# Performance work log

Measured on AMD Instinct MI355X. Metric: run time of the kernel, lower is better.

Reference implementation:

```python
import jax, jax.numpy as jnp
import numpy as np


def setup_inputs() -> dict:
    key = jax.random.key(0)
    kq, kk, kv = jax.random.split(key, 3)
    B, H, S, D = 2, 16, 2048, 128
    return {
        "query_states": jax.random.normal(kq, (B, H, S, D), dtype=jnp.float32),
        "key_states": jax.random.normal(kk, (B, H, S, D), dtype=jnp.float32),
        "value_states": jax.random.normal(kv, (B, H, S, D), dtype=jnp.float32),
    }


def reference(query_states, key_states, value_states):
    # Faithful translation of CoreAttention.forward with attention_mask=None,
    # attention_dropout=0.0 (default, and dropout with p=0 is identity).
    B, H, Sq, D = query_states.shape
    Skv = key_states.shape[-2]
    scale = 1.0 / jnp.sqrt(jnp.asarray(D, dtype=query_states.dtype))
    # [B,H,Sq,Skv] score matrix (the module materializes this explicitly)
    attn_weights = jnp.einsum("bhqd,bhkd->bhqk", query_states, key_states) * scale
    # internal causal mask: triu(ones, diagonal=1) positions -> dtype min
    causal = jnp.triu(jnp.ones((Sq, Skv), dtype=bool), k=1)
    mask_value = jnp.finfo(attn_weights.dtype).min
    attn_weights = jnp.where(causal[None, None], mask_value, attn_weights)
    # torch does softmax in float64 then casts back; numerically stable fp32
    # softmax is equivalent to working precision here (jax x64 disabled).
    attn_weights = jax.nn.softmax(attn_weights, axis=-1).astype(query_states.dtype)
    attn_output = jnp.einsum("bhqk,bhkd->bhqd", attn_weights, value_states)
    return attn_output
```

## Files before the change

### kernel.cpp

```cpp
#include <hip/hip_runtime.h>
#include <hip/hip_bf16.h>
#include <stdint.h>

typedef __bf16  bf16x8 __attribute__((ext_vector_type(8)));
typedef __bf16  bf16x4 __attribute__((ext_vector_type(4)));
typedef float   f32x4  __attribute__((ext_vector_type(4)));
typedef uint32_t u32x4 __attribute__((ext_vector_type(4)));

#define SLEN  2048
#define DHEAD 128
#define QBLK  64
#define KVBLK 32
#define NQT   (SLEN / QBLK)
#define THR   8.0f
#define VSTR  40

__device__ __forceinline__ uint32_t cvt_pk(float lo, float hi2) {
    uint32_t u;
    asm("v_cvt_pk_bf16_f32 %0, %1, %2" : "=v"(u) : "v"(lo), "v"(hi2));
    return u;
}

__global__ __launch_bounds__(256, 3) void attn_fwd(
    const float* __restrict__ Q, const float* __restrict__ K,
    const float* __restrict__ V, float* __restrict__ O)
{
    const int bh = blockIdx.x;
    const int qt = (NQT - 1) - blockIdx.y;
    const int tid  = threadIdx.x;
    const int w    = tid >> 6;
    const int lane = tid & 63;
    const int r    = lane & 15;
    const int g    = lane >> 4;

    const size_t head_off = (size_t)bh * SLEN * DHEAD;
    const float* Qh = Q + head_off;
    const float* Kh = K + head_off;
    const float* Vh = V + head_off;
    float*       Oh = O + head_off;

    const int q0w = qt * QBLK + w * 16;

    __shared__ __bf16 K_sh [2][KVBLK * DHEAD];
    __shared__ __bf16 Vt_sh[2][DHEAD * VSTR];

    const float scale = 0.08838834764831845f;

    bf16x8 qfrag[4];
    {
        const float4* qp = reinterpret_cast<const float4*>(
            Qh + (size_t)(q0w + r) * DHEAD + g * 8);
        #pragma unroll
        for (int kb = 0; kb < 4; ++kb) {
            float4 a = qp[kb*8 + 0];
            float4 b = qp[kb*8 + 1];
            a.x*=scale; a.y*=scale; a.z*=scale; a.w*=scale;
            b.x*=scale; b.y*=scale; b.z*=scale; b.w*=scale;
            bf16x8 f;
            f[0]=(__bf16)a.x; f[1]=(__bf16)a.y; f[2]=(__bf16)a.z; f[3]=(__bf16)a.w;
            f[4]=(__bf16)b.x; f[5]=(__bf16)b.y; f[6]=(__bf16)b.z; f[7]=(__bf16)b.w;
            qfrag[kb] = f;
        }
    }

    float4 kreg[4], vreg[4];
    const int c4  = tid & 31;
    const int kvq = tid >> 5;

    auto issue_loads = [&](int kv0) {
        #pragma unroll
        for (int it = 0; it < 4; ++it) {
            const int row = (it * 256 + tid) >> 5;
            kreg[it] = *reinterpret_cast<const float4*>(
                Kh + (size_t)(kv0 + row) * DHEAD + c4 * 4);
        }
        #pragma unroll
        for (int kr = 0; kr < 4; ++kr)
            vreg[kr] = *reinterpret_cast<const float4*>(
                Vh + (size_t)(kv0 + kvq * 4 + kr) * DHEAD + c4 * 4);
    };

    auto write_tiles = [&](int buf) {
        char* Kb  = reinterpret_cast<char*>(K_sh[buf]);
        char* Vtb = reinterpret_cast<char*>(Vt_sh[buf]);
        #pragma unroll
        for (int it = 0; it < 4; ++it) {
            const int row = (it * 256 + tid) >> 5;
            bf16x4 k4;
            k4[0]=(__bf16)kreg[it].x; k4[1]=(__bf16)kreg[it].y;
            k4[2]=(__bf16)kreg[it].z; k4[3]=(__bf16)kreg[it].w;
            *reinterpret_cast<bf16x4*>(
                Kb + row * 256 + ((c4 * 8) ^ ((row & 15) << 4))) = k4;
        }
        #pragma unroll
        for (int j = 0; j < 4; ++j) {
            const int d = c4 * 4 + j;
            bf16x4 v4;
            #pragma unroll
            for (int kr = 0; kr < 4; ++kr)
                v4[kr] = (__bf16)((&vreg[kr].x)[j]);
            *reinterpret_cast<bf16x4*>(
                Vtb + d * 80 + ((kvq ^ ((d >> 2) & 6)) * 8)) = v4;
        }
    };

    const f32x4 vzero = {0.f, 0.f, 0.f, 0.f};
    f32x4 acc_o[8];
    #pragma unroll
    for (int i = 0; i < 8; ++i) acc_o[i] = vzero;
    float m_run = -1e30f, l_run = 0.f;

    issue_loads(0);
    write_tiles(0);

    const int kvt_blk_max = 2 * qt + 1;
    const int kvt_max_w   = (q0w + 15) >> 5;
    int cur = 0;

    for (int kvt = 0; kvt <= kvt_blk_max; ++kvt) {
        __syncthreads();
        const bool more = (kvt < kvt_blk_max);
        if (more) issue_loads((kvt + 1) * KVBLK);

        if (kvt <= kvt_max_w) {
            const int kv0 = kvt * KVBLK;
            char* Kb  = reinterpret_cast<char*>(K_sh[cur]);
            char* Vtb = reinterpret_cast<char*>(Vt_sh[cur]);

            const bool alive1 = (kv0 + 16 <= q0w + 15);

            f32x4 st[2] = {vzero, vzero};
            __builtin_amdgcn_s_setprio(1);
            #pragma unroll
            for (int t = 0; t < 2; ++t) {
                if (t == 1 && !alive1) break;
                const int row = t * 16 + r;
                #pragma unroll
                for (int kb = 0; kb < 4; ++kb) {
                    bf16x8 kf = *reinterpret_cast<const bf16x8*>(
                        Kb + row * 256 + ((kb*64 + g*16) ^ ((row & 15) << 4)));
                    st[t] = __builtin_amdgcn_mfma_f32_16x16x32_bf16(
                        kf, qfrag[kb], st[t], 0, 0, 0);
                }
            }
            __builtin_amdgcn_s_setprio(0);

            const int q = q0w + r;
            float pmax = -1e30f;
            #pragma unroll
            for (int t = 0; t < 2; ++t) {
                if (t == 1 && !alive1) break;
                if (kv0 + t*16 + 15 > q0w) {
                    #pragma unroll
                    for (int j = 0; j < 4; ++j)
                        if (kv0 + t*16 + 4*g + j > q) st[t][j] = -1e30f;
                }
                #pragma unroll
                for (int j = 0; j < 4; ++j) pmax = fmaxf(pmax, st[t][j]);
            }
            pmax = fmaxf(pmax, __shfl_xor(pmax, 16));
            pmax = fmaxf(pmax, __shfl_xor(pmax, 32));

            if (__any(pmax > m_run + THR)) {
                const float m_new = fmaxf(m_run, pmax);
                const float corr  = __expf(m_run - m_new);
                l_run *= corr; m_run = m_new;
                #pragma unroll
                for (int reg = 0; reg < 4; ++reg) {
                    const float cr = __shfl(corr, 4*g + reg);
                    #pragma unroll
                    for (int dt = 0; dt < 8; ++dt) acc_o[dt][reg] *= cr;
                }
            }

            float rowsum = 0.f;
            #pragma unroll
            for (int t = 0; t < 2; ++t) {
                if (t == 1 && !alive1) break;
                #pragma unroll
                for (int j = 0; j < 4; ++j) {
                    const float p = __expf(st[t][j] - m_run);
                    st[t][j] = p;
                    rowsum += p;
                }
            }
            rowsum += __shfl_xor(rowsum, 16);
            rowsum += __shfl_xor(rowsum, 32);
            l_run += rowsum;

            const uint32_t p00 = cvt_pk(st[0][0], st[0][1]);
            const uint32_t p01 = cvt_pk(st[0][2], st[0][3]);
            const uint32_t p10 = alive1 ? cvt_pk(st[1][0], st[1][1]) : 0u;
            const uint32_t p11 = alive1 ? cvt_pk(st[1][2], st[1][3]) : 0u;
            const int sA = r + ((2 * (g & 1)) << 4);
            const int sB = r + ((2 * (g & 1) + 1) << 4);
            u32x4 words;
            {
                const uint32_t lo0 = (uint32_t)__shfl((int)p00, sA);
                const uint32_t hi0 = (uint32_t)__shfl((int)p10, sA);
                const uint32_t lo1 = (uint32_t)__shfl((int)p01, sA);
                const uint32_t hi1 = (uint32_t)__shfl((int)p11, sA);
                const uint32_t lo2 = (uint32_t)__shfl((int)p00, sB);
                const uint32_t hi2 = (uint32_t)__shfl((int)p10, sB);
                const uint32_t lo3 = (uint32_t)__shfl((int)p01, sB);
                const uint32_t hi3 = (uint32_t)__shfl((int)p11, sB);
                words[0] = (g & 2) ? hi0 : lo0;
                words[1] = (g & 2) ? hi1 : lo1;
                words[2] = (g & 2) ? hi2 : lo2;
                words[3] = (g & 2) ? hi3 : lo3;
            }
            const bf16x8 pa = __builtin_bit_cast(bf16x8, words);

            __builtin_amdgcn_s_setprio(1);
            #pragma unroll
            for (int dt = 0; dt < 8; ++dt) {
                const int d = dt * 16 + r;
                bf16x8 vf = *reinterpret_cast<const bf16x8*>(
                    Vtb + d * 80 + (((2*g) ^ ((d >> 2) & 6)) * 8));
                acc_o[dt] = __builtin_amdgcn_mfma_f32_16x16x32_bf16(
                    pa, vf, acc_o[dt], 0, 0, 0);
            }
            __builtin_amdgcn_s_setprio(0);
        }

        if (more) write_tiles(cur ^ 1);
        cur ^= 1;
    }

    const float inv = 1.0f / l_run;
    #pragma unroll
    for (int reg = 0; reg < 4; ++reg) {
        const float iv = __shfl(inv, 4*g + reg);
        float* orow = Oh + (size_t)(q0w + 4*g + reg) * DHEAD + r;
        #pragma unroll
        for (int dt = 0; dt < 8; ++dt)
            orow[dt * 16] = acc_o[dt][reg] * iv;
    }
}

extern "C" void kernel_launch(void* const* d_in, const int* in_sizes, int n_in,
                              void* d_out, int out_size, void* d_ws, size_t ws_size,
                              hipStream_t stream) {
    const float* Q = (const float*)d_in[0];
    const float* K = (const float*)d_in[1];
    const float* V = (const float*)d_in[2];
    float* O = (float*)d_out;
    dim3 grid(32 , NQT);
    attn_fwd<<<grid, 256, 0, stream>>>(Q, K, V, O);
}
```

Baseline: 92.46 us.

## Split KV range across two warp groups with 512-thread blocks and merge partial softmax

New measurement: 108.0 us. 16.8% more time.

```diff
diff --git a/kernel.cpp b/kernel.cpp
--- a/kernel.cpp
+++ b/kernel.cpp
@@ -10,10 +10,8 @@
 #define SLEN  2048
 #define DHEAD 128
 #define QBLK  64
-#define KVBLK 32
 #define NQT   (SLEN / QBLK)
 #define THR   8.0f
-#define VSTR  40
 
 __device__ __forceinline__ uint32_t cvt_pk(float lo, float hi2) {
     uint32_t u;
@@ -21,7 +19,7 @@
     return u;
 }
 
-__global__ __launch_bounds__(256, 3) void attn_fwd(
+__global__ __launch_bounds__(512, 4) void attn_fwd(
     const float* __restrict__ Q, const float* __restrict__ K,
     const float* __restrict__ V, float* __restrict__ O)
 {
@@ -29,6 +27,8 @@
     const int qt = (NQT - 1) - blockIdx.y;
     const int tid  = threadIdx.x;
     const int w    = tid >> 6;
+    const int tb   = w >> 2;
+    const int wq   = w & 3;
     const int lane = tid & 63;
     const int r    = lane & 15;
     const int g    = lane >> 4;
@@ -39,10 +39,10 @@
     const float* Vh = V + head_off;
     float*       Oh = O + head_off;
 
-    const int q0w = qt * QBLK + w * 16;
-
-    __shared__ __bf16 K_sh [2][KVBLK * DHEAD];
-    __shared__ __bf16 Vt_sh[2][DHEAD * VSTR];
+    const int q0w = qt * QBLK + wq * 16;
+
+    __shared__ __align__(16) char smem[65536];
+    __shared__ float ml_sh[4][16][2];
 
     const float scale = 0.08838834764831845f;
 
@@ -64,28 +64,28 @@
     }
 
     float4 kreg[4], vreg[4];
-    const int c4  = tid & 31;
-    const int kvq = tid >> 5;
+    const int c4 = tid & 31;
+    const int q6 = tid >> 5;
 
     auto issue_loads = [&](int kv0) {
         #pragma unroll
         for (int it = 0; it < 4; ++it) {
-            const int row = (it * 256 + tid) >> 5;
+            const int row = (it * 512 + tid) >> 5;
             kreg[it] = *reinterpret_cast<const float4*>(
                 Kh + (size_t)(kv0 + row) * DHEAD + c4 * 4);
         }
         #pragma unroll
         for (int kr = 0; kr < 4; ++kr)
             vreg[kr] = *reinterpret_cast<const float4*>(
-                Vh + (size_t)(kv0 + kvq * 4 + kr) * DHEAD + c4 * 4);
+                Vh + (size_t)(kv0 + q6 * 4 + kr) * DHEAD + c4 * 4);
     };
 
     auto write_tiles = [&](int buf) {
-        char* Kb  = reinterpret_cast<char*>(K_sh[buf]);
-        char* Vtb = reinterpret_cast<char*>(Vt_sh[buf]);
+        char* Kb  = smem + buf * 16384;
+        char* Vtb = smem + 32768 + buf * 16384;
         #pragma unroll
         for (int it = 0; it < 4; ++it) {
-            const int row = (it * 256 + tid) >> 5;
+            const int row = (it * 512 + tid) >> 5;
             bf16x4 k4;
             k4[0]=(__bf16)kreg[it].x; k4[1]=(__bf16)kreg[it].y;
             k4[2]=(__bf16)kreg[it].z; k4[3]=(__bf16)kreg[it].w;
@@ -99,8 +99,9 @@
             #pragma unroll
             for (int kr = 0; kr < 4; ++kr)
                 v4[kr] = (__bf16)((&vreg[kr].x)[j]);
+            const int slot16 = (q6 >> 1) ^ ((c4 + 2*j) & 7);
             *reinterpret_cast<bf16x4*>(
-                Vtb + d * 80 + ((kvq ^ ((d >> 2) & 6)) * 8)) = v4;
+                Vtb + d * 128 + (slot16 << 4) + ((q6 & 1) << 3)) = v4;
         }
     };
 
@@ -113,20 +114,17 @@
     issue_loads(0);
     write_tiles(0);
 
-    const int kvt_blk_max = 2 * qt + 1;
-    const int kvt_max_w   = (q0w + 15) >> 5;
+    const int n_iter = qt + 1;
     int cur = 0;
 
-    for (int kvt = 0; kvt <= kvt_blk_max; ++kvt) {
+    for (int i = 0; i < n_iter; ++i) {
         __syncthreads();
-        const bool more = (kvt < kvt_blk_max);
-        if (more) issue_loads((kvt + 1) * KVBLK);
-
-        if (kvt <= kvt_max_w) {
-            const int kv0 = kvt * KVBLK;
-            char* Kb  = reinterpret_cast<char*>(K_sh[cur]);
-            char* Vtb = reinterpret_cast<char*>(Vt_sh[cur]);
-
+        if (i + 1 < n_iter) issue_loads((i + 1) * 64);
+
+        const int kv0 = i * 64 + tb * 32;
+        if (kv0 <= q0w + 15) {
+            char* Kb  = smem + cur * 16384;
+            char* Vtb = smem + 32768 + cur * 16384;
             const bool alive1 = (kv0 + 16 <= q0w + 15);
 
             f32x4 st[2] = {vzero, vzero};
@@ -134,11 +132,11 @@
             #pragma unroll
             for (int t = 0; t < 2; ++t) {
                 if (t == 1 && !alive1) break;
-                const int row = t * 16 + r;
+                const int row = tb * 32 + t * 16 + r;
                 #pragma unroll
                 for (int kb = 0; kb < 4; ++kb) {
                     bf16x8 kf = *reinterpret_cast<const bf16x8*>(
-                        Kb + row * 256 + ((kb*64 + g*16) ^ ((row & 15) << 4)));
+                        Kb + row * 256 + ((kb*64 + g*16) ^ (r << 4)));
                     st[t] = __builtin_amdgcn_mfma_f32_16x16x32_bf16(
                         kf, qfrag[kb], st[t], 0, 0, 0);
                 }
@@ -215,26 +213,51 @@
             #pragma unroll
             for (int dt = 0; dt < 8; ++dt) {
                 const int d = dt * 16 + r;
+                const int X = (dt*4 + (r >> 2) + 2*(r & 3)) & 7;
+                const int slot16 = ((tb << 2) + g) ^ X;
                 bf16x8 vf = *reinterpret_cast<const bf16x8*>(
-                    Vtb + d * 80 + (((2*g) ^ ((d >> 2) & 6)) * 8));
+                    Vtb + d * 128 + (slot16 << 4));
                 acc_o[dt] = __builtin_amdgcn_mfma_f32_16x16x32_bf16(
                     pa, vf, acc_o[dt], 0, 0, 0);
             }
             __builtin_amdgcn_s_setprio(0);
         }
 
-        if (more) write_tiles(cur ^ 1);
+        if (i + 1 < n_iter) write_tiles(cur ^ 1);
         cur ^= 1;
     }
 
-    const float inv = 1.0f / l_run;
-    #pragma unroll
-    for (int reg = 0; reg < 4; ++reg) {
-        const float iv = __shfl(inv, 4*g + reg);
-        float* orow = Oh + (size_t)(q0w + 4*g + reg) * DHEAD + r;
-        #pragma unroll
-        for (int dt = 0; dt < 8; ++dt)
-            orow[dt * 16] = acc_o[dt][reg] * iv;
+    __syncthreads();
+    float* Om = reinterpret_cast<float*>(smem);
+    if (tb == 1) {
+        if (g == 0) { ml_sh[wq][r][0] = m_run; ml_sh[wq][r][1] = l_run; }
+        #pragma unroll
+        for (int reg = 0; reg < 4; ++reg) {
+            float* orow = Om + (wq * 16 + 4*g + reg) * 132 + r;
+            #pragma unroll
+            for (int dt = 0; dt < 8; ++dt)
+                orow[dt * 16] = acc_o[dt][reg];
+        }
+    }
+    __syncthreads();
+    if (tb == 0) {
+        #pragma unroll
+        for (int reg = 0; reg < 4; ++reg) {
+            const int ql = 4*g + reg;
+            const float ma = __shfl(m_run, ql);
+            const float la = __shfl(l_run, ql);
+            const float mb = ml_sh[wq][ql][0];
+            const float lb = ml_sh[wq][ql][1];
+            const float ms = fmaxf(ma, mb);
+            const float fa = __expf(ma - ms);
+            const float fb = __expf(mb - ms);
+            const float inv = 1.0f / (la * fa + lb * fb);
+            const float* brow = Om + (wq * 16 + ql) * 132 + r;
+            float* orow = Oh + (size_t)(q0w + ql) * DHEAD + r;
+            #pragma unroll
+            for (int dt = 0; dt < 8; ++dt)
+                orow[dt * 16] = (acc_o[dt][reg] * fa + brow[dt * 16] * fb) * inv;
+        }
     }
 }
 
@@ -246,5 +269,5 @@
     const float* V = (const float*)d_in[2];
     float* O = (float*)d_out;
     dim3 grid(32 , NQT);
-    attn_fwd<<<grid, 256, 0, stream>>>(Q, K, V, O);
+    attn_fwd<<<grid, 512, 0, stream>>>(Q, K, V, O);
 }
```
